# Kernel tuning notes

Hardware: AMD Instinct MI355X
Metric: run time of the kernel (lower is better)

Reference implementation:

```python
import jax, jax.numpy as jnp
import numpy as np

L = 4      # temporal transformer layers
H = 8      # heads
D = 512    # d_model (CLIP ViT-B/32 output dim)
FF = 2048  # feedforward dim
Q = 32     # query_pad_length
NEXP = 2   # visual expansion tokens
EPS = 1e-5


def _l2norm(x):
    n = jnp.linalg.norm(x, axis=-1, keepdims=True)
    return x / jnp.maximum(n, 1e-12)


def _layer_norm(x, w, b):
    m = jnp.mean(x, axis=-1, keepdims=True)
    v = jnp.mean(jnp.square(x - m), axis=-1, keepdims=True)
    return (x - m) / jnp.sqrt(v + EPS) * w + b


def _encoder_layer(x, Wqkv, bqkv, Wo, bo, g1, c1, W1, b1, W2, b2, g2, c2):
    # PyTorch TransformerEncoderLayer, batch_first, post-norm, ReLU, eval mode.
    B, S, _ = x.shape
    dh = D // H
    qkv = x @ Wqkv.T + bqkv                      # [B,S,3D]
    q, k, v = jnp.split(qkv, 3, axis=-1)
    q = q.reshape(B, S, H, dh).transpose(0, 2, 1, 3)
    k = k.reshape(B, S, H, dh).transpose(0, 2, 1, 3)
    v = v.reshape(B, S, H, dh).transpose(0, 2, 1, 3)
    scores = jnp.einsum('bhqd,bhkd->bhqk', q, k) / jnp.sqrt(jnp.float32(dh))
    attn = jax.nn.softmax(scores, axis=-1)
    o = jnp.einsum('bhqk,bhkd->bhqd', attn, v).transpose(0, 2, 1, 3).reshape(B, S, D)
    o = o @ Wo.T + bo
    x = _layer_norm(x + o, g1, c1)
    ff = jax.nn.relu(x @ W1.T + b1) @ W2.T + b2
    x = _layer_norm(x + ff, g2, c2)
    return x


def setup_inputs() -> dict:
    key = jax.random.key(0)
    ks = jax.random.split(key, 8)
    B, F = 256, 30
    s = 0.02
    return {
        'text_features': jax.random.normal(ks[0], (B, D), dtype=jnp.float32),
        'frame_features': jax.random.normal(ks[1], (B, F, D), dtype=jnp.float32),
        'expansion_tokens': jax.random.normal(ks[2], (1, NEXP, D), dtype=jnp.float32) * s,
        'W_qkv': jax.random.normal(ks[3], (L, 3 * D, D), dtype=jnp.float32) * s,
        'b_qkv': jnp.zeros((L, 3 * D), jnp.float32),
        'W_o': jax.random.normal(ks[4], (L, D, D), dtype=jnp.float32) * s,
        'b_o': jnp.zeros((L, D), jnp.float32),
        'ln1_w': jnp.ones((L, D), jnp.float32),
        'ln1_b': jnp.zeros((L, D), jnp.float32),
        'W1': jax.random.normal(ks[5], (L, FF, D), dtype=jnp.float32) * s,
        'b1': jnp.zeros((L, FF), jnp.float32),
        'W2': jax.random.normal(ks[6], (L, D, FF), dtype=jnp.float32) * s,
        'b2': jnp.zeros((L, D), jnp.float32),
        'ln2_w': jnp.ones((L, D), jnp.float32),
        'ln2_b': jnp.zeros((L, D), jnp.float32),
    }


def reference(text_features, frame_features, expansion_tokens, W_qkv, b_qkv,
              W_o, b_o, ln1_w, ln1_b, W1, b1, W2, b2, ln2_w, ln2_b):
    B, F = frame_features.shape[0], frame_features.shape[1]
    # encode_query: expand pooled text feature to Q identical tokens, l2-normalize
    q_feats = _l2norm(jnp.broadcast_to(text_features[:, None, :], (B, Q, D)))
    # temporal encoder on [frames; expansion tokens]
    x = jnp.concatenate(
        [frame_features, jnp.broadcast_to(expansion_tokens, (B, NEXP, D))], axis=1)
    for l in range(L):
        x = _encoder_layer(x, W_qkv[l], b_qkv[l], W_o[l], b_o[l],
                           ln1_w[l], ln1_b[l], W1[l], b1[l], W2[l], b2[l],
                           ln2_w[l], ln2_b[l])
    frame_n = _l2norm(frame_features)   # [B,F,D]
    video_n = _l2norm(x)                # [B,F+NEXP,D]
    # pairwise ColBERT MaxSim: similarities[i,j] = MMS(query_i, video_j)
    sim_f = jnp.einsum('bqd,cfd->bcqf', q_feats, frame_n).max(axis=-1).mean(axis=-1)
    sim_v = jnp.einsum('bqd,cvd->bcqv', q_feats, video_n).max(axis=-1).mean(axis=-1)
    return (sim_f + sim_v, sim_f, sim_v)
```

## Files before the change

### kernel.cpp

```cpp
#include <hip/hip_runtime.h>
#include <math.h>

#define DM 512
#define NTOK_V 62

typedef _Float16 h16;
typedef __attribute__((ext_vector_type(8))) _Float16 h16x8;
typedef __attribute__((ext_vector_type(4))) float f32x4;

__device__ __forceinline__ void ldsload16(const void* g, void* l) {
    __builtin_amdgcn_global_load_lds(
        (const __attribute__((address_space(1))) unsigned int*)g,
        (__attribute__((address_space(3))) unsigned int*)l, 16, 0, 0);
}

__device__ __forceinline__ void xcd_swz(int& bx, int& by) {
    const int gx = gridDim.x, gy = gridDim.y;
    const int lin = blockIdx.x + gx * blockIdx.y;
    const int cpx = (gx * gy) >> 3;
    const int wg = (lin & 7) * cpx + (lin >> 3);
    bx = wg % gx;
    by = wg / gx;
}

__global__ __launch_bounds__(256) void k_cvt(const float* __restrict__ in,
                                             h16* __restrict__ outp, int n8) {
    int i = blockIdx.x * 256 + threadIdx.x;
    if (i >= n8) return;
    float4 a = ((const float4*)in)[i * 2];
    float4 b = ((const float4*)in)[i * 2 + 1];
    h16x8 h;
    h[0] = (h16)a.x; h[1] = (h16)a.y; h[2] = (h16)a.z; h[3] = (h16)a.w;
    h[4] = (h16)b.x; h[5] = (h16)b.y; h[6] = (h16)b.z; h[7] = (h16)b.w;
    ((h16x8*)outp)[i] = h;
}

__global__ __launch_bounds__(256) void k_concat_h(const float* __restrict__ frames,
                                                  const float* __restrict__ expt,
                                                  h16* __restrict__ X) {
    int row = blockIdx.x;
    int b = row >> 5, s = row & 31;
    int t = threadIdx.x;
    const float* src = (s < 30) ? (frames + ((size_t)(b * 30 + s)) * DM)
                                : (expt + (size_t)(s - 30) * DM);
    X[(size_t)row * DM + t]       = (h16)src[t];
    X[(size_t)row * DM + t + 256] = (h16)src[t + 256];
}

template<int MODE>
__global__ __launch_bounds__(512, 2) void k_g8(
        const h16* __restrict__ A, int lda,
        const h16* __restrict__ B, int ldb,
        const float* __restrict__ bias,
        h16* __restrict__ C, int ldc,
        int M, int N, int Keff) {
    __shared__ char smem[131072];
    const int t = threadIdx.x;
    const int w = t >> 6, lane = t & 63;
    const int wr = w >> 2, wc = w & 3;
    const int kc = lane >> 4, rr = lane & 15;
    int bx, by;
    xcd_swz(bx, by);
    const size_t row0 = (size_t)by * 256;
    const size_t col0 = (size_t)bx * 256;

    const h16* gA = A + (row0 + (w << 4) + rr) * (size_t)lda + (kc << 3);
    const h16* gB = B + (col0 + (w << 4) + rr) * (size_t)ldb + (kc << 3);

    f32x4 acc[8][4];
#pragma unroll
    for (int m = 0; m < 8; ++m)
#pragma unroll
        for (int n = 0; n < 4; ++n) acc[m][n] = (f32x4){0.f, 0.f, 0.f, 0.f};

    const int nt = Keff >> 6;

#define SB0 __builtin_amdgcn_sched_barrier(0);
#define STG_A(bs, h, jt) { char* d_ = smem + (bs)*65536 + (h)*16384 + (w << 10) + (lane << 4); \
        const h16* s_ = gA + (size_t)((h)*128) * lda + (size_t)(jt)*64; \
        ldsload16(s_, d_); ldsload16(s_ + 32, d_ + 8192); }
#define STG_B(bs, h, jt) { char* d_ = smem + (bs)*65536 + 32768 + (h)*16384 + (w << 10) + (lane << 4); \
        const h16* s_ = gB + (size_t)((h)*128) * ldb + (size_t)(jt)*64; \
        ldsload16(s_, d_); ldsload16(s_ + 32, d_ + 8192); }
#define MFMA16(mp, AF) { \
        __builtin_amdgcn_s_setprio(1); \
        _Pragma("unroll") for (int i = 0; i < 2; ++i) \
        _Pragma("unroll") for (int n = 0; n < 4; ++n) \
        _Pragma("unroll") for (int kk = 0; kk < 2; ++kk) \
            acc[(mp)*2 + i][n] = __builtin_amdgcn_mfma_f32_16x16x32_f16(AF[i][kk], bf[n][kk], acc[(mp)*2 + i][n], 0, 0, 0); \
        __builtin_amdgcn_s_setprio(0); SB0 }

    STG_A(0, 0, 0) STG_A(0, 1, 0) STG_B(0, 0, 0) STG_B(0, 1, 0)

    int cur = 0;
    for (int j = 0; j < nt; ++j) {
        const int nxt = cur ^ 1;
        if (j + 1 < nt) {
            STG_A(nxt, 0, j + 1)
            asm volatile("s_waitcnt vmcnt(2)" ::: "memory");
        } else {
            asm volatile("s_waitcnt vmcnt(0)" ::: "memory");
        }
        SB0
        __builtin_amdgcn_s_barrier();
        SB0
        const char* Ab = smem + cur * 65536 + wr * 16384;
        const char* Bb = smem + cur * 65536 + 32768 + (wc >> 1) * 16384;
        h16x8 bf[4][2];
#pragma unroll
        for (int n = 0; n < 4; ++n)
#pragma unroll
            for (int kk = 0; kk < 2; ++kk)
                bf[n][kk] = *(const h16x8*)(Bb + kk * 8192 + (((wc & 1) << 2) + n) * 1024 + (lane << 4));
        h16x8 a0[2][2];
#pragma unroll
        for (int i = 0; i < 2; ++i)
#pragma unroll
            for (int kk = 0; kk < 2; ++kk)
                a0[i][kk] = *(const h16x8*)(Ab + kk * 8192 + (0 + i) * 1024 + (lane << 4));
        asm volatile("s_waitcnt lgkmcnt(0)" ::: "memory");
        SB0
        MFMA16(0, a0)
        h16x8 a1[2][2];
#pragma unroll
        for (int i = 0; i < 2; ++i)
#pragma unroll
            for (int kk = 0; kk < 2; ++kk)
                a1[i][kk] = *(const h16x8*)(Ab + kk * 8192 + (2 + i) * 1024 + (lane << 4));
        if (j + 1 < nt) STG_A(nxt, 1, j + 1)
        asm volatile("s_waitcnt lgkmcnt(0)" ::: "memory");
        SB0
        __builtin_amdgcn_s_barrier();
        SB0
        MFMA16(1, a1)
        h16x8 a2[2][2];
#pragma unroll
        for (int i = 0; i < 2; ++i)
#pragma unroll
            for (int kk = 0; kk < 2; ++kk)
                a2[i][kk] = *(const h16x8*)(Ab + kk * 8192 + (4 + i) * 1024 + (lane << 4));
        if (j + 1 < nt) STG_B(nxt, 0, j + 1)
        asm volatile("s_waitcnt lgkmcnt(0)" ::: "memory");
        SB0
        __builtin_amdgcn_s_barrier();
        SB0
        MFMA16(2, a2)
        h16x8 a3[2][2];
#pragma unroll
        for (int i = 0; i < 2; ++i)
#pragma unroll
            for (int kk = 0; kk < 2; ++kk)
                a3[i][kk] = *(const h16x8*)(Ab + kk * 8192 + (6 + i) * 1024 + (lane << 4));
        if (j + 1 < nt) STG_B(nxt, 1, j + 1)
        asm volatile("s_waitcnt lgkmcnt(0)" ::: "memory");
        SB0
        __builtin_amdgcn_s_barrier();
        SB0
        MFMA16(3, a3)
        cur = nxt;
    }
#undef MFMA16
#undef STG_A
#undef STG_B
#undef SB0

    float bv[4];
#pragma unroll
    for (int n = 0; n < 4; ++n)
        bv[n] = bias ? bias[col0 + (wc << 6) + n * 16 + rr] : 0.f;
#pragma unroll
    for (int m = 0; m < 8; ++m) {
        size_t rbase = row0 + (wr << 7) + m * 16 + (kc << 2);
#pragma unroll
        for (int jj = 0; jj < 4; ++jj) {
            h16* rowp = C + (rbase + jj) * (size_t)ldc + col0 + (wc << 6) + rr;
#pragma unroll
            for (int n = 0; n < 4; ++n) {
                float v = acc[m][n][jj] + bv[n];
                if (MODE == 1) v = fmaxf(v, 0.f);
                rowp[n * 16] = (h16)v;
            }
        }
    }
}

__global__ __launch_bounds__(512, 2) void k_g8n(
        const h16* __restrict__ A, int lda,
        const h16* __restrict__ B, int ldb,
        h16* __restrict__ C, int ldc,
        int M, int N, int Keff) {
    __shared__ char smem[98304];
    const int t = threadIdx.x;
    const int w = t >> 6, lane = t & 63;
    const int wr = w >> 1, wc = w & 1;
    const int kc = lane >> 4, rr = lane & 15;
    int bx, by;
    xcd_swz(bx, by);
    const size_t row0 = (size_t)by * 256;
    const size_t col0 = (size_t)bx * 128;
    const int z = blockIdx.z;

    const h16* gA = A + (size_t)z * Keff + (row0 + (w << 4) + rr) * (size_t)lda + (kc << 3);
    const h16* gB = B + (size_t)z * Keff + (col0 + (w << 4) + rr) * (size_t)ldb + (kc << 3);
    h16* Cz = C + (size_t)z * (size_t)M * N;

    f32x4 acc[4][4];
#pragma unroll
    for (int m = 0; m < 4; ++m)
#pragma unroll
        for (int n = 0; n < 4; ++n) acc[m][n] = (f32x4){0.f, 0.f, 0.f, 0.f};

    const int nt = Keff >> 6;

#define SB0 __builtin_amdgcn_sched_barrier(0);
#define STG_A(bs, h, jt) { char* d_ = smem + (bs)*49152 + (h)*16384 + (w << 10) + (lane << 4); \
        const h16* s_ = gA + (size_t)((h)*128) * lda + (size_t)(jt)*64; \
        ldsload16(s_, d_); ldsload16(s_ + 32, d_ + 8192); }
#define STG_B(bs, jt) { char* d_ = smem + (bs)*49152 + 32768 + (w << 10) + (lane << 4); \
        const h16* s_ = gB + (size_t)(jt)*64; \
        ldsload16(s_, d_); ldsload16(s_ + 32, d_ + 8192); }
#define MFMA8(mp, AF) { \
        __builtin_amdgcn_s_setprio(1); \
        _Pragma("unroll") for (int n = 0; n < 4; ++n) \
        _Pragma("unroll") for (int kk = 0; kk < 2; ++kk) \
            acc[mp][n] = __builtin_amdgcn_mfma_f32_16x16x32_f16(AF[kk], bf[n][kk], acc[mp][n], 0, 0, 0); \
        __builtin_amdgcn_s_setprio(0); SB0 }
#define LDA_FRAG(dst, mp) { int g_ = (wr << 2) + (mp); \
        const char* p_ = smem + cur * 49152 + ((g_ >> 3) << 14) + ((g_ & 7) << 10) + (lane << 4); \
        _Pragma("unroll") for (int kk = 0; kk < 2; ++kk) \
            dst[kk] = *(const h16x8*)(p_ + kk * 8192); }

    STG_A(0, 0, 0) STG_A(0, 1, 0) STG_B(0, 0)

    int cur = 0;
    for (int j = 0; j < nt; ++j) {
        const int nxt = cur ^ 1;
        if (j + 1 < nt) {
            STG_A(nxt, 0, j + 1)
            asm volatile("s_waitcnt vmcnt(2)" ::: "memory");
        } else {
            asm volatile("s_waitcnt vmcnt(0)" ::: "memory");
        }
        SB0
        __builtin_amdgcn_s_barrier();
        SB0
        const char* Bb = smem + cur * 49152 + 32768;
        h16x8 bf[4][2];
#pragma unroll
        for (int n = 0; n < 4; ++n)
#pragma unroll
            for (int kk = 0; kk < 2; ++kk)
                bf[n][kk] = *(const h16x8*)(Bb + kk * 8192 + (((wc << 2) + n) << 10) + (lane << 4));
        h16x8 a0[2];
        LDA_FRAG(a0, 0)
        asm volatile("s_waitcnt lgkmcnt(0)" ::: "memory");
        SB0
        MFMA8(0, a0)
        h16x8 a1[2];
        LDA_FRAG(a1, 1)
        if (j + 1 < nt) STG_A(nxt, 1, j + 1)
        asm volatile("s_waitcnt lgkmcnt(0)" ::: "memory");
        SB0
        __builtin_amdgcn_s_barrier();
        SB0
        MFMA8(1, a1)
        h16x8 a2[2];
        LDA_FRAG(a2, 2)
        if (j + 1 < nt) STG_B(nxt, j + 1)
        asm volatile("s_waitcnt lgkmcnt(0)" ::: "memory");
        SB0
        __builtin_amdgcn_s_barrier();
        SB0
        MFMA8(2, a2)
        h16x8 a3[2];
        LDA_FRAG(a3, 3)
        asm volatile("s_waitcnt lgkmcnt(0)" ::: "memory");
        SB0
        __builtin_amdgcn_s_barrier();
        SB0
        MFMA8(3, a3)
        cur = nxt;
    }
#undef LDA_FRAG
#undef MFMA8
#undef STG_A
#undef STG_B
#undef SB0

#pragma unroll
    for (int m = 0; m < 4; ++m) {
        size_t rbase = row0 + (wr << 6) + m * 16 + (kc << 2);
#pragma unroll
        for (int jj = 0; jj < 4; ++jj) {
            h16* rowp = Cz + (rbase + jj) * (size_t)ldc + col0 + (wc << 6) + rr;
#pragma unroll
            for (int n = 0; n < 4; ++n)
                rowp[n * 16] = (h16)acc[m][n][jj];
        }
    }
}

template<int MODE>
__global__ __launch_bounds__(512, 4) void k_hgemm(
        const h16* __restrict__ A, int lda,
        const h16* __restrict__ B, int ldb,
        const float* __restrict__ bias,
        h16* __restrict__ C, int ldc,
        int M, int N, int Keff) {
    __shared__ char smem[49152];
    const int t = threadIdx.x;
    const int w = t >> 6, lane = t & 63;
    const int wr = w >> 2, wc = w & 3;
    const int kc = lane >> 4, rr = lane & 15;
    int bx, by;
    xcd_swz(bx, by);
    const size_t row0 = (size_t)by * 128;
    const size_t col0 = (size_t)bx * 128;

    const h16* gA = A + (row0 + (w << 4) + rr) * (size_t)lda + (kc << 3);
    const h16* gB = B + (col0 + (w << 4) + rr) * (size_t)ldb + (kc << 3);

    f32x4 acc[4][2];
#pragma unroll
    for (int m = 0; m < 4; ++m)
#pragma unroll
        for (int n = 0; n < 2; ++n) acc[m][n] = (f32x4){0.f, 0.f, 0.f, 0.f};

    const int nt = Keff >> 5;

#define SB0 __builtin_amdgcn_sched_barrier(0);
#define STAGE(step, slot) { char* sA_ = smem + ((slot) << 14) + (w << 10); \
        ldsload16(gA + (size_t)(step) * 32, sA_); \
        ldsload16(gB + (size_t)(step) * 32, sA_ + 8192); }
#define KSTEP(WAITLIT, slotR, DOSTAGE, stepW, slotW) { \
        asm volatile("s_waitcnt vmcnt(" WAITLIT ")" ::: "memory"); \
        SB0 \
        __builtin_amdgcn_s_barrier(); \
        SB0 \
        const char* bA = smem + ((slotR) << 14); \
        const char* bB = bA + 8192; \
        h16x8 af[4], bf[2]; \
        _Pragma("unroll") for (int m = 0; m < 4; ++m) \
            af[m] = *(const h16x8*)(bA + ((wr << 2) + m) * 1024 + lane * 16); \
        _Pragma("unroll") for (int n = 0; n < 2; ++n) \
            bf[n] = *(const h16x8*)(bB + ((wc << 1) + n) * 1024 + lane * 16); \
        asm volatile("s_waitcnt lgkmcnt(0)" ::: "memory"); \
        SB0 \
        if (DOSTAGE) STAGE(stepW, slotW) \
        __builtin_amdgcn_s_setprio(1); \
        _Pragma("unroll") for (int m = 0; m < 4; ++m) \
        _Pragma("unroll") for (int n = 0; n < 2; ++n) \
            acc[m][n] = __builtin_amdgcn_mfma_f32_16x16x32_f16(af[m], bf[n], acc[m][n], 0, 0, 0); \
        __builtin_amdgcn_s_setprio(0); \
        SB0 }

    STAGE(0, 0) STAGE(1, 1)
    int slotR = 0, slotW = 2;
    int it = 0;
    for (; it < nt - 2; ++it) {
        KSTEP("2", slotR, 1, it + 2, slotW)
        slotR = (slotR == 2) ? 0 : slotR + 1;
        slotW = (slotW == 2) ? 0 : slotW + 1;
    }
    KSTEP("2", slotR, 0, 0, 0)
    slotR = (slotR == 2) ? 0 : slotR + 1;
    KSTEP("0", slotR, 0, 0, 0)
#undef KSTEP
#undef STAGE
#undef SB0

#pragma unroll
    for (int n = 0; n < 2; ++n) {
        size_t col = col0 + (wc << 5) + n * 16 + rr;
#pragma unroll
        for (int m = 0; m < 4; ++m) {
            size_t rbase = row0 + (wr << 6) + m * 16 + (kc << 2);
#pragma unroll
            for (int j = 0; j < 4; ++j)
                C[(rbase + j) * (size_t)ldc + col] = (h16)acc[m][n][j];
        }
    }
}

__global__ __launch_bounds__(512, 2) void k_attproj(
        const h16* __restrict__ ATT,
        const h16* __restrict__ Bw,
        const float* __restrict__ bo,
        h16* __restrict__ X,
        const float* __restrict__ lw,
        const float* __restrict__ lb) {
    __shared__ char smem[131072];
    const int t = threadIdx.x;
    const int w = t >> 6, lane = t & 63;
    const int kc = lane >> 4, rr = lane & 15;
    const size_t row0 = (size_t)blockIdx.x * 32;
    const h16* Ain = ATT + row0 * DM;

    f32x4 acc[2][4];
#pragma unroll
    for (int m = 0; m < 2; ++m)
#pragma unroll
        for (int n = 0; n < 4; ++n) acc[m][n] = (f32x4){0.f, 0.f, 0.f, 0.f};

#define SB0 __builtin_amdgcn_sched_barrier(0);
#define STGB(js, sl) { _Pragma("unroll") for (int u = 0; u < 4; ++u) { \
        const h16* s_ = Bw + (size_t)((((u << 3) + w) << 4) + rr) * DM + (js) * 32 + (kc << 3); \
        ldsload16(s_, smem + 32768 + (sl) * 32768 + ((((u << 3) + w) << 10)) + (lane << 4)); } }

#pragma unroll
    for (int u = 0; u < 4; ++u) {
        int sidx = (u << 2) + (w >> 1);
        const h16* s_ = Ain + (size_t)(((w & 1) << 4) + rr) * DM + sidx * 32 + (kc << 3);
        ldsload16(s_, smem + (sidx << 11) + ((w & 1) << 10) + (lane << 4));
    }
    STGB(0, 0) STGB(1, 1)

    int slotR = 0, slotW = 2;
    for (int s = 0; s < 15; ++s) {
        asm volatile("s_waitcnt vmcnt(4)" ::: "memory");
        SB0
        __builtin_amdgcn_s_barrier();
        SB0
        h16x8 af[2], bf[4];
#pragma unroll
        for (int m = 0; m < 2; ++m)
            af[m] = *(const h16x8*)(smem + (s << 11) + (m << 10) + (lane << 4));
#pragma unroll
        for (int n = 0; n < 4; ++n)
            bf[n] = *(const h16x8*)(smem + 32768 + slotR * 32768 + (((w << 2) + n) << 10) + (lane << 4));
        asm volatile("s_waitcnt lgkmcnt(0)" ::: "memory");
        SB0
        if (s + 2 < 16) STGB(s + 2, slotW)
        __builtin_amdgcn_s_setprio(1);
#pragma unroll
        for (int m = 0; m < 2; ++m)
#pragma unroll
            for (int n = 0; n < 4; ++n)
                acc[m][n] = __builtin_amdgcn_mfma_f32_16x16x32_f16(af[m], bf[n], acc[m][n], 0, 0, 0);
        __builtin_amdgcn_s_setprio(0);
        SB0
        slotR = (slotR == 2) ? 0 : slotR + 1;
        slotW = (slotW == 2) ? 0 : slotW + 1;
    }
    {
        asm volatile("s_waitcnt vmcnt(0)" ::: "memory");
        SB0
        __builtin_amdgcn_s_barrier();
        SB0
        h16x8 af[2], bf[4];
#pragma unroll
        for (int m = 0; m < 2; ++m)
            af[m] = *(const h16x8*)(smem + (15 << 11) + (m << 10) + (lane << 4));
#pragma unroll
        for (int n = 0; n < 4; ++n)
            bf[n] = *(const h16x8*)(smem + 32768 + slotR * 32768 + (((w << 2) + n) << 10) + (lane << 4));
        asm volatile("s_waitcnt lgkmcnt(0)" ::: "memory");
        SB0
#pragma unroll
        for (int m = 0; m < 2; ++m)
#pragma unroll
            for (int n = 0; n < 4; ++n)
                acc[m][n] = __builtin_amdgcn_mfma_f32_16x16x32_f16(af[m], bf[n], acc[m][n], 0, 0, 0);
    }
#undef STGB
#undef SB0
    __syncthreads();

    float* outl = (float*)smem;
    float bv[4];
#pragma unroll
    for (int n = 0; n < 4; ++n)
        bv[n] = bo[(w << 6) + n * 16 + rr];
#pragma unroll
    for (int m = 0; m < 2; ++m)
#pragma unroll
        for (int n = 0; n < 4; ++n)
#pragma unroll
            for (int j = 0; j < 4; ++j) {
                int r = m * 16 + (lane >> 4) * 4 + j;
                int c = (w << 6) + n * 16 + rr;
                outl[r * 516 + c] = acc[m][n][j] + bv[n];
            }
    __syncthreads();

    {
        const int r = t >> 4, l = t & 15;
        const size_t grow = (row0 + r) * (size_t)DM;
        float v[32];
        float sum = 0.f, sq = 0.f;
#pragma unroll
        for (int i = 0; i < 32; ++i) {
            int col = l + (i << 4);
            float vv = outl[r * 516 + col] + (float)X[grow + col];
            v[i] = vv;
            sum += vv;
            sq += vv * vv;
        }
#pragma unroll
        for (int o = 8; o; o >>= 1) {
            sum += __shfl_xor(sum, o);
            sq  += __shfl_xor(sq, o);
        }
        float mean = sum * (1.f / 512.f);
        float var = sq * (1.f / 512.f) - mean * mean;
        float inv = 1.f / sqrtf(var + 1e-5f);
#pragma unroll
        for (int i = 0; i < 32; ++i) {
            int col = l + (i << 4);
            X[grow + col] = (h16)((v[i] - mean) * inv * lw[col] + lb[col]);
        }
    }
}

__global__ __launch_bounds__(256) void k_attn_h(const h16* __restrict__ qkv,
                                                h16* __restrict__ att) {
    __shared__ float q[32][65], k[32][65], v[32][65];
    __shared__ float sc[32][33];
    int b = blockIdx.x >> 3, h = blockIdx.x & 7;
    int t = threadIdx.x;
    const h16* base = qkv + (size_t)b * 32 * 1536 + h * 64;
    for (int i = t; i < 2048; i += 256) {
        int s = i >> 6, d = i & 63;
        size_t ro = (size_t)s * 1536 + d;
        q[s][d] = (float)base[ro];
        k[s][d] = (float)base[ro + 512];
        v[s][d] = (float)base[ro + 1024];
    }
    __syncthreads();
    {
        int r = t >> 3, c0 = (t & 7) << 2;
        float s0 = 0.f, s1 = 0.f, s2 = 0.f, s3 = 0.f;
#pragma unroll 8
        for (int d = 0; d < 64; ++d) {
            float qv = q[r][d];
            s0 += qv * k[c0 + 0][d];
            s1 += qv * k[c0 + 1][d];
            s2 += qv * k[c0 + 2][d];
            s3 += qv * k[c0 + 3][d];
        }
        sc[r][c0 + 0] = s0 * 0.125f;
        sc[r][c0 + 1] = s1 * 0.125f;
        sc[r][c0 + 2] = s2 * 0.125f;
        sc[r][c0 + 3] = s3 * 0.125f;
    }
    __syncthreads();
    {
        int r = t >> 3, c0 = (t & 7) << 2;
        float a0 = sc[r][c0], a1 = sc[r][c0 + 1], a2 = sc[r][c0 + 2], a3 = sc[r][c0 + 3];
        float mx = fmaxf(fmaxf(a0, a1), fmaxf(a2, a3));
        mx = fmaxf(mx, __shfl_xor(mx, 1));
        mx = fmaxf(mx, __shfl_xor(mx, 2));
        mx = fmaxf(mx, __shfl_xor(mx, 4));
        float e0 = expf(a0 - mx), e1 = expf(a1 - mx), e2 = expf(a2 - mx), e3 = expf(a3 - mx);
        float sm = e0 + e1 + e2 + e3;
        sm += __shfl_xor(sm, 1);
        sm += __shfl_xor(sm, 2);
        sm += __shfl_xor(sm, 4);
        float inv = 1.f / sm;
        sc[r][c0] = e0 * inv; sc[r][c0 + 1] = e1 * inv; sc[r][c0 + 2] = e2 * inv; sc[r][c0 + 3] = e3 * inv;
    }
    __syncthreads();
    for (int i = t; i < 2048; i += 256) {
        int s = i >> 6, d = i & 63;
        float acc = 0.f;
#pragma unroll 8
        for (int c = 0; c < 32; ++c) acc += sc[s][c] * v[c][d];
        att[((size_t)b * 32 + s) * DM + h * 64 + d] = (h16)acc;
    }
}

__global__ __launch_bounds__(256) void k_addln_red(h16* __restrict__ x,
                                                   const h16* __restrict__ p0,
                                                   const h16* __restrict__ p1,
                                                   const float* __restrict__ bias,
                                                   const float* __restrict__ w,
                                                   const float* __restrict__ b) {
    size_t row = blockIdx.x;
    int t = threadIdx.x;
    size_t o0 = row * DM + t, o1 = o0 + 256;
    float v0 = (float)x[o0] + (float)p0[o0] + (float)p1[o0] + bias[t];
    float v1 = (float)x[o1] + (float)p0[o1] + (float)p1[o1] + bias[t + 256];
    float s = v0 + v1;
#pragma unroll
    for (int o = 32; o; o >>= 1) s += __shfl_xor(s, o);
    __shared__ float ss[4], qs[4];
    if ((t & 63) == 0) ss[t >> 6] = s;
    __syncthreads();
    float mean = (ss[0] + ss[1] + ss[2] + ss[3]) * (1.f / 512.f);
    float d0 = v0 - mean, d1 = v1 - mean;
    float qv = d0 * d0 + d1 * d1;
#pragma unroll
    for (int o = 32; o; o >>= 1) qv += __shfl_xor(qv, o);
    if ((t & 63) == 0) qs[t >> 6] = qv;
    __syncthreads();
    float var = (qs[0] + qs[1] + qs[2] + qs[3]) * (1.f / 512.f);
    float inv = 1.f / sqrtf(var + 1e-5f);
    x[o0] = (h16)(d0 * inv * w[t] + b[t]);
    x[o1] = (h16)(d1 * inv * w[t + 256] + b[t + 256]);
}

__global__ __launch_bounds__(256) void k_l2rows_h(const float* __restrict__ in,
                                                  h16* __restrict__ outp) {
    size_t row = blockIdx.x;
    int t = threadIdx.x;
    float v0 = in[row * DM + t], v1 = in[row * DM + t + 256];
    float q = v0 * v0 + v1 * v1;
#pragma unroll
    for (int o = 32; o; o >>= 1) q += __shfl_xor(q, o);
    __shared__ float qs[4];
    if ((t & 63) == 0) qs[t >> 6] = q;
    __syncthreads();
    float n = sqrtf(qs[0] + qs[1] + qs[2] + qs[3]);
    float sc = 1.f / fmaxf(n, 1e-12f);
    outp[row * DM + t]       = (h16)(v0 * sc);
    outp[row * DM + t + 256] = (h16)(v1 * sc);
}

__global__ __launch_bounds__(256) void k_build_tok_h(const float* __restrict__ frames,
                                                     const h16* __restrict__ X,
                                                     h16* __restrict__ TOK) {
    int rid = blockIdx.x;
    int j = rid / NTOK_V, tt = rid % NTOK_V;
    int t = threadIdx.x;
    float v0, v1;
    if (tt < 30) {
        const float* src = frames + ((size_t)j * 30 + tt) * DM;
        v0 = src[t]; v1 = src[t + 256];
    } else {
        const h16* src = X + ((size_t)j * 32 + (tt - 30)) * DM;
        v0 = (float)src[t]; v1 = (float)src[t + 256];
    }
    float q = v0 * v0 + v1 * v1;
#pragma unroll
    for (int o = 32; o; o >>= 1) q += __shfl_xor(q, o);
    __shared__ float qs[4];
    if ((t & 63) == 0) qs[t >> 6] = q;
    __syncthreads();
    float n = sqrtf(qs[0] + qs[1] + qs[2] + qs[3]);
    float sc = 1.f / fmaxf(n, 1e-12f);
    TOK[(size_t)rid * DM + t]       = (h16)(v0 * sc);
    TOK[(size_t)rid * DM + t + 256] = (h16)(v1 * sc);
}

__global__ __launch_bounds__(256) void k_sim_h(const h16* __restrict__ dots,
                                               float* __restrict__ out) {
    int i = blockIdx.x;
    int j = threadIdx.x;
    const h16* p = dots + (size_t)i * 15872 + (size_t)j * NTOK_V;
    float mf = -1e30f, mv = -1e30f;
#pragma unroll
    for (int tt = 0; tt < 30; ++tt) mf = fmaxf(mf, (float)p[tt]);
#pragma unroll
    for (int tt = 30; tt < 62; ++tt) mv = fmaxf(mv, (float)p[tt]);
    int o = i * 256 + j;
    out[o]          = mf + mv;
    out[65536 + o]  = mf;
    out[131072 + o] = mv;
}

extern "C" void kernel_launch(void* const* d_in, const int* in_sizes, int n_in,
                              void* d_out, int out_size, void* d_ws, size_t ws_size,
                              hipStream_t stream) {
    const float* text   = (const float*)d_in[0];
    const float* frames = (const float*)d_in[1];
    const float* expt   = (const float*)d_in[2];
    const float* Wqkv   = (const float*)d_in[3];
    const float* bqkv   = (const float*)d_in[4];
    const float* Wo     = (const float*)d_in[5];
    const float* bo     = (const float*)d_in[6];
    const float* ln1w   = (const float*)d_in[7];
    const float* ln1b   = (const float*)d_in[8];
    const float* W1     = (const float*)d_in[9];
    const float* b1     = (const float*)d_in[10];
    const float* W2     = (const float*)d_in[11];
    const float* b2     = (const float*)d_in[12];
    const float* ln2w   = (const float*)d_in[13];
    const float* ln2b   = (const float*)d_in[14];
    float* out = (float*)d_out;

    char* wsb = (char*)d_ws;
    const size_t MB = 1024 * 1024;
    h16* Xh    = (h16*)(wsb);
    h16* P0    = (h16*)(wsb + 8 * MB);
    h16* P1    = (h16*)(wsb + 16 * MB);
    h16* ATTh  = (h16*)(wsb + 24 * MB);
    h16* FFh   = (h16*)(wsb + 32 * MB);
    h16* TOKh  = (h16*)(wsb + 32 * MB);
    h16* DOTSh = (h16*)(wsb + 48 * MB);
    h16* Wh    = (h16*)(wsb + 64 * MB);
    h16* QHATh = (h16*)(wsb + 90 * MB);

    h16* Whqkv = Wh;
    h16* Who   = Whqkv + 3145728;
    h16* Wh1   = Who + 1048576;
    h16* Wh2   = Wh1 + 4194304;

    k_cvt<<<1536, 256, 0, stream>>>(Wqkv, Whqkv, 393216);
    k_cvt<<<512,  256, 0, stream>>>(Wo,   Who,   131072);
    k_cvt<<<2048, 256, 0, stream>>>(W1,   Wh1,   524288);
    k_cvt<<<2048, 256, 0, stream>>>(W2,   Wh2,   524288);
    k_concat_h<<<8192, 256, 0, stream>>>(frames, expt, Xh);

    for (int l = 0; l < 4; ++l) {
        const h16* Wqkv_l = Whqkv + (size_t)l * 786432;
        const h16* Wo_l   = Who   + (size_t)l * 262144;
        const h16* W1_l   = Wh1   + (size_t)l * 1048576;
        const h16* W2_l   = Wh2   + (size_t)l * 1048576;

        k_g8<0><<<dim3(6, 32, 1), 512, 0, stream>>>(
            Xh, 512, Wqkv_l, 512, bqkv + (size_t)l * 1536, FFh, 1536, 8192, 1536, 512);
        k_attn_h<<<2048, 256, 0, stream>>>(FFh, ATTh);
        k_attproj<<<256, 512, 0, stream>>>(ATTh, Wo_l, bo + (size_t)l * 512, Xh,
                                           ln1w + (size_t)l * 512, ln1b + (size_t)l * 512);
        k_g8<1><<<dim3(8, 32, 1), 512, 0, stream>>>(
            Xh, 512, W1_l, 512, b1 + (size_t)l * 2048, FFh, 2048, 8192, 2048, 512);
        k_g8n<<<dim3(4, 32, 2), 512, 0, stream>>>(
            FFh, 2048, W2_l, 2048, P0, 512, 8192, 512, 1024);
        k_addln_red<<<8192, 256, 0, stream>>>(Xh, P0, P1, b2 + (size_t)l * 512,
                                              ln2w + (size_t)l * 512, ln2b + (size_t)l * 512);
    }

    k_l2rows_h<<<256, 256, 0, stream>>>(text, QHATh);
    k_build_tok_h<<<256 * NTOK_V, 256, 0, stream>>>(frames, Xh, TOKh);
    k_hgemm<2><<<dim3(124, 2, 1), 512, 0, stream>>>(
        QHATh, 512, TOKh, 512, nullptr, DOTSh, 15872, 256, 15872, 512);
    k_sim_h<<<256, 256, 0, stream>>>(DOTSh, out);
}
```

Before: 609.8 us.

## Fuse per-head MFMA attention into output projection and LayerNorm kernel

Replaces the scalar fp32 attention kernel and the separate attention-projection kernel with one kernel per batch element. Each of the 8 waves computes one head's QK^T, softmax and PV with f16 MFMA instructions. The attention output is written straight into LDS as the A operand of the Wo GEMM, which is followed by the residual add and LayerNorm. This removes a kernel launch and the global round trip of the attention output, and moves the attention math onto the matrix cores. In exchange, launch bounds drop to one block per CU, and the V operand is gathered element by element from LDS.

```diff
diff --git a/kernel.cpp b/kernel.cpp
--- a/kernel.cpp
+++ b/kernel.cpp
@@ -382,9 +382,9 @@
     }
 }
 
-__global__ __launch_bounds__(512, 2) void k_attproj(
-        const h16* __restrict__ ATT,
-        const h16* __restrict__ Bw,
+__global__ __launch_bounds__(512, 1) void k_fattn(
+        const h16* __restrict__ QKV,
+        const h16* __restrict__ Wo,
         const float* __restrict__ bo,
         h16* __restrict__ X,
         const float* __restrict__ lw,
@@ -392,9 +392,115 @@
     __shared__ char smem[131072];
     const int t = threadIdx.x;
     const int w = t >> 6, lane = t & 63;
-    const int kc = lane >> 4, rr = lane & 15;
-    const size_t row0 = (size_t)blockIdx.x * 32;
-    const h16* Ain = ATT + row0 * DM;
+    const int rr = lane & 15, kc = lane >> 4;
+    const size_t b = blockIdx.x;
+    const size_t row0 = b * 32;
+    const h16* qkv = QKV + row0 * 1536;
+
+#define SB0 __builtin_amdgcn_sched_barrier(0);
+#pragma unroll
+    for (int mat = 0; mat < 3; ++mat)
+#pragma unroll
+        for (int g = 0; g < 2; ++g)
+#pragma unroll
+            for (int q = 0; q < 2; ++q) {
+                const h16* src = qkv + (size_t)(g * 16 + rr) * 1536 + mat * 512 + w * 64 + q * 32 + kc * 8;
+                ldsload16(src, smem + w * 12288 + mat * 4096 + (g * 2 + q) * 1024 + lane * 16);
+            }
+    asm volatile("s_waitcnt vmcnt(4)" ::: "memory");
+    SB0
+
+    const char* Qb = smem + w * 12288;
+    const char* Kb = Qb + 4096;
+    f32x4 s[2][2];
+#pragma unroll
+    for (int m = 0; m < 2; ++m)
+#pragma unroll
+        for (int n = 0; n < 2; ++n) s[m][n] = (f32x4){0.f, 0.f, 0.f, 0.f};
+#pragma unroll
+    for (int q = 0; q < 2; ++q) {
+        h16x8 aq[2], bk[2];
+#pragma unroll
+        for (int m = 0; m < 2; ++m) aq[m] = *(const h16x8*)(Qb + (m * 2 + q) * 1024 + lane * 16);
+#pragma unroll
+        for (int n = 0; n < 2; ++n) bk[n] = *(const h16x8*)(Kb + (n * 2 + q) * 1024 + lane * 16);
+#pragma unroll
+        for (int m = 0; m < 2; ++m)
+#pragma unroll
+            for (int n = 0; n < 2; ++n)
+                s[m][n] = __builtin_amdgcn_mfma_f32_16x16x32_f16(aq[m], bk[n], s[m][n], 0, 0, 0);
+    }
+
+    float p[2][2][4];
+#pragma unroll
+    for (int m = 0; m < 2; ++m)
+#pragma unroll
+        for (int j = 0; j < 4; ++j) {
+            float a0 = s[m][0][j] * 0.125f, a1 = s[m][1][j] * 0.125f;
+            float mx = fmaxf(a0, a1);
+            mx = fmaxf(mx, __shfl_xor(mx, 1));
+            mx = fmaxf(mx, __shfl_xor(mx, 2));
+            mx = fmaxf(mx, __shfl_xor(mx, 4));
+            mx = fmaxf(mx, __shfl_xor(mx, 8));
+            float e0 = expf(a0 - mx), e1 = expf(a1 - mx);
+            float sm = e0 + e1;
+            sm += __shfl_xor(sm, 1);
+            sm += __shfl_xor(sm, 2);
+            sm += __shfl_xor(sm, 4);
+            sm += __shfl_xor(sm, 8);
+            float inv = 1.f / sm;
+            p[m][0][j] = e0 * inv;
+            p[m][1][j] = e1 * inv;
+        }
+
+    char* Pb = smem + 98304 + w * 2048;
+#pragma unroll
+    for (int m = 0; m < 2; ++m)
+#pragma unroll
+        for (int n = 0; n < 2; ++n)
+#pragma unroll
+            for (int j = 0; j < 4; ++j)
+                *(h16*)(Pb + m * 1024 + (kc * 4 + j + ((n * 2 + (rr >> 3)) & 3) * 16) * 16 + (lane & 7) * 2) = (h16)p[m][n][j];
+    asm volatile("s_waitcnt lgkmcnt(0)" ::: "memory");
+    SB0
+    h16x8 ap[2];
+#pragma unroll
+    for (int m = 0; m < 2; ++m) ap[m] = *(const h16x8*)(Pb + m * 1024 + lane * 16);
+
+    asm volatile("s_waitcnt vmcnt(0)" ::: "memory");
+    SB0
+
+    const char* Vb = Qb + 8192;
+    f32x4 o[2][4];
+#pragma unroll
+    for (int m = 0; m < 2; ++m)
+#pragma unroll
+        for (int n = 0; n < 4; ++n) o[m][n] = (f32x4){0.f, 0.f, 0.f, 0.f};
+#pragma unroll
+    for (int n = 0; n < 4; ++n) {
+        h16x8 bv;
+#pragma unroll
+        for (int e = 0; e < 8; ++e)
+            bv[e] = *(const h16*)(Vb + ((kc >> 1) * 2 + (n >> 1)) * 1024
+                                  + ((kc & 1) * 8 + e) * 16
+                                  + ((n * 2 + (rr >> 3)) & 3) * 256 + (lane & 7) * 2);
+#pragma unroll
+        for (int m = 0; m < 2; ++m)
+            o[m][n] = __builtin_amdgcn_mfma_f32_16x16x32_f16(ap[m], bv, o[m][n], 0, 0, 0);
+    }
+
+#pragma unroll
+    for (int m = 0; m < 2; ++m)
+#pragma unroll
+        for (int n = 0; n < 4; ++n)
+#pragma unroll
+            for (int j = 0; j < 4; ++j)
+                *(h16*)(smem + 98304 + (m * 16 + w * 2 + (n >> 1)) * 1024
+                        + (kc * 4 + j + ((n & 1) * 2 + (rr >> 3)) * 16) * 16 + (lane & 7) * 2) = (h16)o[m][n][j];
+    asm volatile("s_waitcnt lgkmcnt(0)" ::: "memory");
+    SB0
+    __builtin_amdgcn_s_barrier();
+    SB0
 
     f32x4 acc[2][4];
 #pragma unroll
@@ -402,21 +508,13 @@
 #pragma unroll
         for (int n = 0; n < 4; ++n) acc[m][n] = (f32x4){0.f, 0.f, 0.f, 0.f};
 
-#define SB0 __builtin_amdgcn_sched_barrier(0);
 #define STGB(js, sl) { _Pragma("unroll") for (int u = 0; u < 4; ++u) { \
-        const h16* s_ = Bw + (size_t)((((u << 3) + w) << 4) + rr) * DM + (js) * 32 + (kc << 3); \
-        ldsload16(s_, smem + 32768 + (sl) * 32768 + ((((u << 3) + w) << 10)) + (lane << 4)); } }
-
-#pragma unroll
-    for (int u = 0; u < 4; ++u) {
-        int sidx = (u << 2) + (w >> 1);
-        const h16* s_ = Ain + (size_t)(((w & 1) << 4) + rr) * DM + sidx * 32 + (kc << 3);
-        ldsload16(s_, smem + (sidx << 11) + ((w & 1) << 10) + (lane << 4));
-    }
+        const h16* s_ = Wo + (size_t)((((u << 3) + w) << 4) + rr) * DM + (js) * 32 + (kc << 3); \
+        ldsload16(s_, smem + (sl) * 32768 + (((u << 3) + w) << 10) + (lane << 4)); } }
+
     STGB(0, 0) STGB(1, 1)
-
     int slotR = 0, slotW = 2;
-    for (int s = 0; s < 15; ++s) {
+    for (int sx = 0; sx < 15; ++sx) {
         asm volatile("s_waitcnt vmcnt(4)" ::: "memory");
         SB0
         __builtin_amdgcn_s_barrier();
@@ -424,13 +522,13 @@
         h16x8 af[2], bf[4];
 #pragma unroll
         for (int m = 0; m < 2; ++m)
-            af[m] = *(const h16x8*)(smem + (s << 11) + (m << 10) + (lane << 4));
+            af[m] = *(const h16x8*)(smem + 98304 + (m * 16 + sx) * 1024 + (lane << 4));
 #pragma unroll
         for (int n = 0; n < 4; ++n)
-            bf[n] = *(const h16x8*)(smem + 32768 + slotR * 32768 + (((w << 2) + n) << 10) + (lane << 4));
-        asm volatile("s_waitcnt lgkmcnt(0)" ::: "memory");
-        SB0
-        if (s + 2 < 16) STGB(s + 2, slotW)
+            bf[n] = *(const h16x8*)(smem + slotR * 32768 + (((w << 2) + n) << 10) + (lane << 4));
+        asm volatile("s_waitcnt lgkmcnt(0)" ::: "memory");
+        SB0
+        if (sx + 2 < 16) STGB(sx + 2, slotW)
         __builtin_amdgcn_s_setprio(1);
 #pragma unroll
         for (int m = 0; m < 2; ++m)
@@ -450,10 +548,10 @@
         h16x8 af[2], bf[4];
 #pragma unroll
         for (int m = 0; m < 2; ++m)
-            af[m] = *(const h16x8*)(smem + (15 << 11) + (m << 10) + (lane << 4));
+            af[m] = *(const h16x8*)(smem + 98304 + (m * 16 + 15) * 1024 + (lane << 4));
 #pragma unroll
         for (int n = 0; n < 4; ++n)
-            bf[n] = *(const h16x8*)(smem + 32768 + slotR * 32768 + (((w << 2) + n) << 10) + (lane << 4));
+            bf[n] = *(const h16x8*)(smem + slotR * 32768 + (((w << 2) + n) << 10) + (lane << 4));
         asm volatile("s_waitcnt lgkmcnt(0)" ::: "memory");
         SB0
 #pragma unroll
@@ -467,22 +565,21 @@
     __syncthreads();
 
     float* outl = (float*)smem;
-    float bv[4];
+    float bvv[4];
 #pragma unroll
     for (int n = 0; n < 4; ++n)
-        bv[n] = bo[(w << 6) + n * 16 + rr];
+        bvv[n] = bo[(w << 6) + n * 16 + rr];
 #pragma unroll
     for (int m = 0; m < 2; ++m)
 #pragma unroll
         for (int n = 0; n < 4; ++n)
 #pragma unroll
             for (int j = 0; j < 4; ++j) {
-                int r = m * 16 + (lane >> 4) * 4 + j;
+                int r = m * 16 + kc * 4 + j;
                 int c = (w << 6) + n * 16 + rr;
-                outl[r * 516 + c] = acc[m][n][j] + bv[n];
+                outl[r * 516 + c] = acc[m][n][j] + bvv[n];
             }
     __syncthreads();
-
     {
         const int r = t >> 4, l = t & 15;
         const size_t grow = (row0 + r) * (size_t)DM;
@@ -497,9 +594,9 @@
             sq += vv * vv;
         }
 #pragma unroll
-        for (int o = 8; o; o >>= 1) {
-            sum += __shfl_xor(sum, o);
-            sq  += __shfl_xor(sq, o);
+        for (int o2 = 8; o2; o2 >>= 1) {
+            sum += __shfl_xor(sum, o2);
+            sq  += __shfl_xor(sq, o2);
         }
         float mean = sum * (1.f / 512.f);
         float var = sq * (1.f / 512.f) - mean * mean;
@@ -509,63 +606,6 @@
             int col = l + (i << 4);
             X[grow + col] = (h16)((v[i] - mean) * inv * lw[col] + lb[col]);
         }
-    }
-}
-
-__global__ __launch_bounds__(256) void k_attn_h(const h16* __restrict__ qkv,
-                                                h16* __restrict__ att) {
-    __shared__ float q[32][65], k[32][65], v[32][65];
-    __shared__ float sc[32][33];
-    int b = blockIdx.x >> 3, h = blockIdx.x & 7;
-    int t = threadIdx.x;
-    const h16* base = qkv + (size_t)b * 32 * 1536 + h * 64;
-    for (int i = t; i < 2048; i += 256) {
-        int s = i >> 6, d = i & 63;
-        size_t ro = (size_t)s * 1536 + d;
-        q[s][d] = (float)base[ro];
-        k[s][d] = (float)base[ro + 512];
-        v[s][d] = (float)base[ro + 1024];
-    }
-    __syncthreads();
-    {
-        int r = t >> 3, c0 = (t & 7) << 2;
-        float s0 = 0.f, s1 = 0.f, s2 = 0.f, s3 = 0.f;
-#pragma unroll 8
-        for (int d = 0; d < 64; ++d) {
-            float qv = q[r][d];
-            s0 += qv * k[c0 + 0][d];
-            s1 += qv * k[c0 + 1][d];
-            s2 += qv * k[c0 + 2][d];
-            s3 += qv * k[c0 + 3][d];
-        }
-        sc[r][c0 + 0] = s0 * 0.125f;
-        sc[r][c0 + 1] = s1 * 0.125f;
-        sc[r][c0 + 2] = s2 * 0.125f;
-        sc[r][c0 + 3] = s3 * 0.125f;
-    }
-    __syncthreads();
-    {
-        int r = t >> 3, c0 = (t & 7) << 2;
-        float a0 = sc[r][c0], a1 = sc[r][c0 + 1], a2 = sc[r][c0 + 2], a3 = sc[r][c0 + 3];
-        float mx = fmaxf(fmaxf(a0, a1), fmaxf(a2, a3));
-        mx = fmaxf(mx, __shfl_xor(mx, 1));
-        mx = fmaxf(mx, __shfl_xor(mx, 2));
-        mx = fmaxf(mx, __shfl_xor(mx, 4));
-        float e0 = expf(a0 - mx), e1 = expf(a1 - mx), e2 = expf(a2 - mx), e3 = expf(a3 - mx);
-        float sm = e0 + e1 + e2 + e3;
-        sm += __shfl_xor(sm, 1);
-        sm += __shfl_xor(sm, 2);
-        sm += __shfl_xor(sm, 4);
-        float inv = 1.f / sm;
-        sc[r][c0] = e0 * inv; sc[r][c0 + 1] = e1 * inv; sc[r][c0 + 2] = e2 * inv; sc[r][c0 + 3] = e3 * inv;
-    }
-    __syncthreads();
-    for (int i = t; i < 2048; i += 256) {
-        int s = i >> 6, d = i & 63;
-        float acc = 0.f;
-#pragma unroll 8
-        for (int c = 0; c < 32; ++c) acc += sc[s][c] * v[c][d];
-        att[((size_t)b * 32 + s) * DM + h * 64 + d] = (h16)acc;
     }
 }
 
@@ -683,7 +723,6 @@
     h16* Xh    = (h16*)(wsb);
     h16* P0    = (h16*)(wsb + 8 * MB);
     h16* P1    = (h16*)(wsb + 16 * MB);
-    h16* ATTh  = (h16*)(wsb + 24 * MB);
     h16* FFh   = (h16*)(wsb + 32 * MB);
     h16* TOKh  = (h16*)(wsb + 32 * MB);
     h16* DOTSh = (h16*)(wsb + 48 * MB);
@@ -709,9 +748,8 @@
 
         k_g8<0><<<dim3(6, 32, 1), 512, 0, stream>>>(
             Xh, 512, Wqkv_l, 512, bqkv + (size_t)l * 1536, FFh, 1536, 8192, 1536, 512);
-        k_attn_h<<<2048, 256, 0, stream>>>(FFh, ATTh);
-        k_attproj<<<256, 512, 0, stream>>>(ATTh, Wo_l, bo + (size_t)l * 512, Xh,
-                                           ln1w + (size_t)l * 512, ln1b + (size_t)l * 512);
+        k_fattn<<<256, 512, 0, stream>>>(FFh, Wo_l, bo + (size_t)l * 512, Xh,
+                                         ln1w + (size_t)l * 512, ln1b + (size_t)l * 512);
         k_g8<1><<<dim3(8, 32, 1), 512, 0, stream>>>(
             Xh, 512, W1_l, 512, b1 + (size_t)l * 2048, FFh, 2048, 8192, 2048, 512);
         k_g8n<<<dim3(4, 32, 2), 512, 0, stream>>>(
```

Result: faster. 516.0 us (-15.4%).
